# Performance work log

Measured on AMD Instinct MI355X. Metric: run time of the kernel, lower is better.

The kernel has to match this reference:

```python
import jax, jax.numpy as jnp
import numpy as np

N_NODES = 100000
N_EDGES = 1250000
D_FEAT = 64


def setup_inputs() -> dict:
    key = jax.random.key(0)
    k1, k2 = jax.random.split(key)
    x = jax.random.normal(k1, (N_NODES, D_FEAT), dtype=jnp.float32)
    edge_index = jax.random.randint(k2, (2, N_EDGES), 0, N_NODES, dtype=jnp.int64)
    return {"t": 0, "x": x, "edge_index": edge_index}


def reference(t, x, edge_index):
    # LGConv(normalize=False): out[i] = sum_{(j->i) in E} x[j]
    # adj_t SpMM expressed as gather + segment-sum scatter.
    src = edge_index[0]  # source/neighbor nodes
    dst = edge_index[1]  # destination nodes
    msgs = x[src]  # [E, D] gather
    out = jax.ops.segment_sum(msgs, dst, num_segments=N_NODES)  # [N, D]
    return out
```

## Files before the change

kernel.cpp:

```cpp
#include <hip/hip_runtime.h>

#define N_NODES 100000
#define N_EDGES 1250000
#define D_FEAT 64

#define NB_SHIFT 7
#define NODES_PER_B 128
#define N_BUCKETS ((N_NODES + NODES_PER_B - 1) / NODES_PER_B)
#define TROW (N_BUCKETS + 1)
#define NB_PAD 1024
#define MAX_BUCKET_EDGES 2048
#define SRC_BITS 17
#define SRC_MASK ((1u << SRC_BITS) - 1u)

#define CH 4992
#define NCH ((N_EDGES + CH - 1) / CH)
#define NCHP 256

__global__ __launch_bounds__(256) void lgconv_scatter(
    const float* __restrict__ x, const int* __restrict__ src,
    const int* __restrict__ dst, float* __restrict__ out) {
    int tid  = blockIdx.x * blockDim.x + threadIdx.x;
    int edge = tid >> 4;
    int f4   = (tid & 15) << 2;
    if (edge >= N_EDGES) return;
    int s = src[edge], d = dst[edge];
    const float4 v = *reinterpret_cast<const float4*>(x + (size_t)s * D_FEAT + f4);
    float* o = out + (size_t)d * D_FEAT + f4;
    unsafeAtomicAdd(o + 0, v.x); unsafeAtomicAdd(o + 1, v.y);
    unsafeAtomicAdd(o + 2, v.z); unsafeAtomicAdd(o + 3, v.w);
}

__device__ __forceinline__ unsigned short f2bf(float f) {
    unsigned int u = __float_as_uint(f);
    return (unsigned short)((u + 0x7FFFu + ((u >> 16) & 1u)) >> 16);
}
__device__ __forceinline__ float bflo(unsigned int p) {
    return __uint_as_float(p << 16);
}
__device__ __forceinline__ float bfhi(unsigned int p) {
    return __uint_as_float(p & 0xFFFF0000u);
}

__device__ __forceinline__ int wscan_incl(int v) {
    const int lane = threadIdx.x & 63;
#pragma unroll
    for (int off = 1; off < 64; off <<= 1) {
        int u = __shfl_up(v, off, 64);
        if (lane >= off) v += u;
    }
    return v;
}

template <bool CONV>
__global__ __launch_bounds__(1024) void k1_sort(
    const float* __restrict__ x, unsigned short* __restrict__ xb,
    const int* __restrict__ src, const int* __restrict__ dst,
    unsigned int* __restrict__ bins, unsigned short* __restrict__ tableT) {
    __shared__ int hist[NB_PAD];
    __shared__ int scanBase[NB_PAD];
    __shared__ int cur[NB_PAD];
    __shared__ int wsum[16];
    __shared__ unsigned int stage[CH];
    const int t    = threadIdx.x;
    const int c    = blockIdx.x;
    const int base = c * CH;
    const int cnt  = min(CH, N_EDGES - base);
    const int lane = t & 63;
    const int wid  = t >> 6;

    if (CONV) {
        const int F4 = N_NODES * D_FEAT / 4;
        for (int i = c * 1024 + t; i < F4; i += NCH * 1024) {
            float4 v = reinterpret_cast<const float4*>(x)[i];
            ushort4 o;
            o.x = f2bf(v.x); o.y = f2bf(v.y); o.z = f2bf(v.z); o.w = f2bf(v.w);
            reinterpret_cast<ushort4*>(xb)[i] = o;
        }
    }

    hist[t] = 0; cur[t] = 0;
    __syncthreads();
    for (int i = t; i < cnt; i += 1024)
        atomicAdd(&hist[dst[base + i] >> NB_SHIFT], 1);
    __syncthreads();

    int v = hist[t];
    int s = wscan_incl(v);
    if (lane == 63) wsum[wid] = s;
    __syncthreads();
    if (t < 16) {
        int w  = wsum[t];
        int ws = wscan_incl(w);
        wsum[t] = ws;
    }
    __syncthreads();
    int incl = s + (wid ? wsum[wid - 1] : 0);
    scanBase[t] = incl - v;
    __syncthreads();

    if (t < TROW) tableT[(size_t)t * NCHP + c] = (unsigned short)scanBase[t];

    for (int i = t; i < cnt; i += 1024) {
        int d = dst[base + i], sv = src[base + i];
        int b = d >> NB_SHIFT;
        unsigned int packed = ((unsigned int)(d & (NODES_PER_B - 1)) << SRC_BITS)
                            | (unsigned int)sv;
        int pos = scanBase[b] + atomicAdd(&cur[b], 1);
        stage[pos] = packed;
    }
    __syncthreads();
    for (int i = t; i < cnt; i += 1024) bins[base + i] = stage[i];
}

template <bool BF>
__global__ __launch_bounds__(512) void k2_accum(
    const float* __restrict__ x, const unsigned short* __restrict__ xb,
    const unsigned int* __restrict__ bins, const unsigned short* __restrict__ tableT,
    float* __restrict__ out) {
    __shared__ int            startA[512];
    __shared__ unsigned short lenA[512];
    __shared__ int            destB[512];
    __shared__ unsigned int   raw[MAX_BUCKET_EDGES];
    __shared__ unsigned int   srcs[MAX_BUCKET_EDGES];
    __shared__ int cntArr[NODES_PER_B];
    __shared__ int nodeOff[NODES_PER_B + 1];
    __shared__ int curN[NODES_PER_B];
    __shared__ int wsum[8];
    const int t    = threadIdx.x;
    const int b    = blockIdx.x;
    const int lane = t & 63;
    const int wid  = t >> 6;

    int st = 0, len = 0;
    if (t < NCH) {
        st  = tableT[(size_t)b * NCHP + t];
        len = (int)tableT[(size_t)(b + 1) * NCHP + t] - st;
    }
    startA[t] = st;
    lenA[t]   = (unsigned short)len;
    if (t < NODES_PER_B) cntArr[t] = 0;
    int s = wscan_incl(len);
    if (lane == 63) wsum[wid] = s;
    __syncthreads();
    if (t < 8) {
        int w  = wsum[t];
        int ws = wscan_incl(w);
        wsum[t] = ws;
    }
    __syncthreads();
    int incl = s + (wid ? wsum[wid - 1] : 0);
    destB[t] = incl - len;
    int cntTot = wsum[7];
    if (cntTot > MAX_BUCKET_EDGES) cntTot = MAX_BUCKET_EDGES;
    __syncthreads();

    {
        const int cj = t >> 3;
        const int jj = t & 7;
        for (int c0 = 0; c0 < NCH; c0 += 64) {
            int c = c0 + cj;
            if (c < NCH) {
                int l = lenA[c], s0 = startA[c], db = destB[c];
                const unsigned int* p = bins + (size_t)c * CH + s0;
                for (int q = jj; q < l; q += 8) raw[db + q] = p[q];
            }
        }
    }
    __syncthreads();

    for (int i = t; i < cntTot; i += 512)
        atomicAdd(&cntArr[raw[i] >> SRC_BITS], 1);
    __syncthreads();
    int v2 = (t < NODES_PER_B) ? cntArr[t] : 0;
    int s2 = wscan_incl(v2);
    if (t < NODES_PER_B && lane == 63) wsum[wid] = s2;
    __syncthreads();
    if (t < NODES_PER_B) {
        int excl = s2 + ((wid == 1) ? wsum[0] : 0) - v2;
        nodeOff[t] = excl;
        curN[t]    = excl;
    }
    if (t == 0) nodeOff[NODES_PER_B] = cntTot;
    __syncthreads();
    for (int i = t; i < cntTot; i += 512) {
        unsigned int p = raw[i];
        int pos = atomicAdd(&curN[p >> SRC_BITS], 1);
        srcs[pos] = p & SRC_MASK;
    }
    __syncthreads();

    if (BF) {
        int f0 = (t & 7) << 3;
        for (int g = 0; g < NODES_PER_B / 64; ++g) {
            int local = g * 64 + (t >> 3);
            int node  = b * NODES_PER_B + local;
            int beg = nodeOff[local], end = nodeOff[local + 1];
            float a0=0,a1=0,a2=0,a3=0,a4=0,a5=0,a6=0,a7=0;
            int k = beg;
            for (; k + 3 < end; k += 4) {
                const uint4 u0 = *reinterpret_cast<const uint4*>(
                    xb + (size_t)srcs[k] * D_FEAT + f0);
                const uint4 u1 = *reinterpret_cast<const uint4*>(
                    xb + (size_t)srcs[k + 1] * D_FEAT + f0);
                const uint4 u2 = *reinterpret_cast<const uint4*>(
                    xb + (size_t)srcs[k + 2] * D_FEAT + f0);
                const uint4 u3 = *reinterpret_cast<const uint4*>(
                    xb + (size_t)srcs[k + 3] * D_FEAT + f0);
                a0 += bflo(u0.x) + bflo(u1.x) + bflo(u2.x) + bflo(u3.x);
                a1 += bfhi(u0.x) + bfhi(u1.x) + bfhi(u2.x) + bfhi(u3.x);
                a2 += bflo(u0.y) + bflo(u1.y) + bflo(u2.y) + bflo(u3.y);
                a3 += bfhi(u0.y) + bfhi(u1.y) + bfhi(u2.y) + bfhi(u3.y);
                a4 += bflo(u0.z) + bflo(u1.z) + bflo(u2.z) + bflo(u3.z);
                a5 += bfhi(u0.z) + bfhi(u1.z) + bfhi(u2.z) + bfhi(u3.z);
                a6 += bflo(u0.w) + bflo(u1.w) + bflo(u2.w) + bflo(u3.w);
                a7 += bfhi(u0.w) + bfhi(u1.w) + bfhi(u2.w) + bfhi(u3.w);
            }
            for (; k < end; ++k) {
                const uint4 u = *reinterpret_cast<const uint4*>(
                    xb + (size_t)srcs[k] * D_FEAT + f0);
                a0 += bflo(u.x); a1 += bfhi(u.x);
                a2 += bflo(u.y); a3 += bfhi(u.y);
                a4 += bflo(u.z); a5 += bfhi(u.z);
                a6 += bflo(u.w); a7 += bfhi(u.w);
            }
            if (node < N_NODES) {
                float* op = out + (size_t)node * D_FEAT + f0;
                *reinterpret_cast<float4*>(op)     = make_float4(a0, a1, a2, a3);
                *reinterpret_cast<float4*>(op + 4) = make_float4(a4, a5, a6, a7);
            }
        }
    } else {
        int lane4 = (t & 15) << 2;
        for (int g = 0; g < NODES_PER_B / 32; ++g) {
            int local = g * 32 + (t >> 4);
            int node  = b * NODES_PER_B + local;
            int beg = nodeOff[local], end = nodeOff[local + 1];
            float4 acc = make_float4(0.f, 0.f, 0.f, 0.f);
            int k = beg;
            for (; k + 1 < end; k += 2) {
                unsigned int i0 = srcs[k], i1 = srcs[k + 1];
                const float4 a = *reinterpret_cast<const float4*>(x + (size_t)i0 * D_FEAT + lane4);
                const float4 c = *reinterpret_cast<const float4*>(x + (size_t)i1 * D_FEAT + lane4);
                acc.x += a.x + c.x; acc.y += a.y + c.y;
                acc.z += a.z + c.z; acc.w += a.w + c.w;
            }
            if (k < end) {
                unsigned int i0 = srcs[k];
                const float4 a = *reinterpret_cast<const float4*>(x + (size_t)i0 * D_FEAT + lane4);
                acc.x += a.x; acc.y += a.y; acc.z += a.z; acc.w += a.w;
            }
            if (node < N_NODES)
                *reinterpret_cast<float4*>(out + (size_t)node * D_FEAT + lane4) = acc;
        }
    }
}

extern "C" void kernel_launch(void* const* d_in, const int* in_sizes, int n_in,
                              void* d_out, int out_size, void* d_ws, size_t ws_size,
                              hipStream_t stream) {
    const float* x   = (const float*)d_in[1];
    const int*   ei  = (const int*)d_in[2];
    const int*   src = ei;
    const int*   dst = ei + N_EDGES;
    float*       out = (float*)d_out;

    const size_t tabBytes = (size_t)TROW * NCHP * sizeof(unsigned short);
    const size_t binBytes = (size_t)N_EDGES * sizeof(unsigned int);
    const size_t xbOff    = (binBytes + tabBytes + 15) & ~(size_t)15;
    const size_t needA    = xbOff + (size_t)N_NODES * D_FEAT * sizeof(unsigned short);
    const size_t needB    = binBytes + tabBytes;

    if (ws_size >= needA) {
        unsigned int*   bins   = (unsigned int*)d_ws;
        unsigned short* tableT = (unsigned short*)((char*)d_ws + binBytes);
        unsigned short* xb     = (unsigned short*)((char*)d_ws + xbOff);
        k1_sort<true><<<NCH, 1024, 0, stream>>>(x, xb, src, dst, bins, tableT);
        k2_accum<true><<<N_BUCKETS, 512, 0, stream>>>(x, xb, bins, tableT, out);
    } else if (ws_size >= needB) {
        unsigned int*   bins   = (unsigned int*)d_ws;
        unsigned short* tableT = (unsigned short*)((char*)d_ws + binBytes);
        k1_sort<false><<<NCH, 1024, 0, stream>>>(x, nullptr, src, dst, bins, tableT);
        k2_accum<false><<<N_BUCKETS, 512, 0, stream>>>(x, nullptr, bins, tableT, out);
    } else {
        hipMemsetAsync(out, 0, (size_t)out_size * sizeof(float), stream);
        const int total = N_EDGES * 16;
        lgconv_scatter<<<(total + 255) / 256, 256, 0, stream>>>(x, src, dst, out);
    }
}
```

Measured before the change: 134.5 us.

## Halve bucket size and split each node's neighbor list across two thread groups

```diff
diff --git a/kernel.cpp b/kernel.cpp
--- a/kernel.cpp
+++ b/kernel.cpp
@@ -4,12 +4,12 @@
 #define N_EDGES 1250000
 #define D_FEAT 64
 
-#define NB_SHIFT 7
-#define NODES_PER_B 128
+#define NB_SHIFT 6
+#define NODES_PER_B 64
 #define N_BUCKETS ((N_NODES + NODES_PER_B - 1) / NODES_PER_B)
 #define TROW (N_BUCKETS + 1)
-#define NB_PAD 1024
-#define MAX_BUCKET_EDGES 2048
+#define NB_PAD 2048
+#define MAX_BUCKET_EDGES 1280
 #define SRC_BITS 17
 #define SRC_MASK ((1u << SRC_BITS) - 1u)
 
@@ -79,14 +79,16 @@
         }
     }
 
-    hist[t] = 0; cur[t] = 0;
+    hist[t] = 0; hist[t + 1024] = 0;
+    cur[t]  = 0; cur[t + 1024]  = 0;
     __syncthreads();
     for (int i = t; i < cnt; i += 1024)
         atomicAdd(&hist[dst[base + i] >> NB_SHIFT], 1);
     __syncthreads();
 
-    int v = hist[t];
-    int s = wscan_incl(v);
+    int v0 = hist[2 * t], v1 = hist[2 * t + 1];
+    int pv = v0 + v1;
+    int s  = wscan_incl(pv);
     if (lane == 63) wsum[wid] = s;
     __syncthreads();
     if (t < 16) {
@@ -96,10 +98,13 @@
     }
     __syncthreads();
     int incl = s + (wid ? wsum[wid - 1] : 0);
-    scanBase[t] = incl - v;
-    __syncthreads();
-
-    if (t < TROW) tableT[(size_t)t * NCHP + c] = (unsigned short)scanBase[t];
+    int eb   = incl - pv;
+    scanBase[2 * t]     = eb;
+    scanBase[2 * t + 1] = eb + v0;
+    __syncthreads();
+
+    for (int i = t; i < TROW; i += 1024)
+        tableT[(size_t)i * NCHP + c] = (unsigned short)scanBase[i];
 
     for (int i = t; i < cnt; i += 1024) {
         int d = dst[base + i], sv = src[base + i];
@@ -156,14 +161,14 @@
     __syncthreads();
 
     {
-        const int cj = t >> 3;
-        const int jj = t & 7;
-        for (int c0 = 0; c0 < NCH; c0 += 64) {
+        const int cj = t >> 2;
+        const int jj = t & 3;
+        for (int c0 = 0; c0 < NCH; c0 += 128) {
             int c = c0 + cj;
             if (c < NCH) {
                 int l = lenA[c], s0 = startA[c], db = destB[c];
                 const unsigned int* p = bins + (size_t)c * CH + s0;
-                for (int q = jj; q < l; q += 8) raw[db + q] = p[q];
+                for (int q = jj; q < l; q += 4) raw[db + q] = p[q];
             }
         }
     }
@@ -172,16 +177,13 @@
     for (int i = t; i < cntTot; i += 512)
         atomicAdd(&cntArr[raw[i] >> SRC_BITS], 1);
     __syncthreads();
-    int v2 = (t < NODES_PER_B) ? cntArr[t] : 0;
-    int s2 = wscan_incl(v2);
-    if (t < NODES_PER_B && lane == 63) wsum[wid] = s2;
-    __syncthreads();
     if (t < NODES_PER_B) {
-        int excl = s2 + ((wid == 1) ? wsum[0] : 0) - v2;
-        nodeOff[t] = excl;
-        curN[t]    = excl;
-    }
-    if (t == 0) nodeOff[NODES_PER_B] = cntTot;
+        int v2 = cntArr[t];
+        int s2 = wscan_incl(v2);
+        nodeOff[t] = s2 - v2;
+        curN[t]    = s2 - v2;
+        if (t == 0) nodeOff[NODES_PER_B] = cntTot;
+    }
     __syncthreads();
     for (int i = t; i < cntTot; i += 512) {
         unsigned int p = raw[i];
@@ -191,14 +193,18 @@
     __syncthreads();
 
     if (BF) {
-        int f0 = (t & 7) << 3;
-        for (int g = 0; g < NODES_PER_B / 64; ++g) {
-            int local = g * 64 + (t >> 3);
+        const int f0  = (t & 7) << 3;
+        const int grp = (t >> 3) & 1;
+        for (int g = 0; g < NODES_PER_B / 32; ++g) {
+            int local = g * 32 + (t >> 4);
             int node  = b * NODES_PER_B + local;
             int beg = nodeOff[local], end = nodeOff[local + 1];
+            int half = (end - beg + 1) >> 1;
+            int b0 = grp ? (beg + half) : beg;
+            int e0 = grp ? end : (beg + half);
             float a0=0,a1=0,a2=0,a3=0,a4=0,a5=0,a6=0,a7=0;
-            int k = beg;
-            for (; k + 3 < end; k += 4) {
+            int k = b0;
+            for (; k + 3 < e0; k += 4) {
                 const uint4 u0 = *reinterpret_cast<const uint4*>(
                     xb + (size_t)srcs[k] * D_FEAT + f0);
                 const uint4 u1 = *reinterpret_cast<const uint4*>(
@@ -216,7 +222,7 @@
                 a6 += bflo(u0.w) + bflo(u1.w) + bflo(u2.w) + bflo(u3.w);
                 a7 += bfhi(u0.w) + bfhi(u1.w) + bfhi(u2.w) + bfhi(u3.w);
             }
-            for (; k < end; ++k) {
+            for (; k < e0; ++k) {
                 const uint4 u = *reinterpret_cast<const uint4*>(
                     xb + (size_t)srcs[k] * D_FEAT + f0);
                 a0 += bflo(u.x); a1 += bfhi(u.x);
@@ -224,7 +230,11 @@
                 a4 += bflo(u.z); a5 += bfhi(u.z);
                 a6 += bflo(u.w); a7 += bfhi(u.w);
             }
-            if (node < N_NODES) {
+            a0 += __shfl_xor(a0, 8, 64); a1 += __shfl_xor(a1, 8, 64);
+            a2 += __shfl_xor(a2, 8, 64); a3 += __shfl_xor(a3, 8, 64);
+            a4 += __shfl_xor(a4, 8, 64); a5 += __shfl_xor(a5, 8, 64);
+            a6 += __shfl_xor(a6, 8, 64); a7 += __shfl_xor(a7, 8, 64);
+            if (grp == 0 && node < N_NODES) {
                 float* op = out + (size_t)node * D_FEAT + f0;
                 *reinterpret_cast<float4*>(op)     = make_float4(a0, a1, a2, a3);
                 *reinterpret_cast<float4*>(op + 4) = make_float4(a4, a5, a6, a7);
```

New measurement: 136.2 us. Within noise of the previous version (+1.2%).

## Split bf16 feature table into quarter slabs and gather per quarter with lane reduction

Applied to the files above, without the earlier changes.

```diff
diff --git a/kernel.cpp b/kernel.cpp
--- a/kernel.cpp
+++ b/kernel.cpp
@@ -16,6 +16,12 @@
 #define CH 4992
 #define NCH ((N_EDGES + CH - 1) / CH)
 #define NCHP 256
+
+#define QFEAT 16
+#define QS_US4 (N_NODES * 4)
+#define QS_US  (N_NODES * QFEAT)
+
+typedef float f32x4 __attribute__((ext_vector_type(4)));
 
 __global__ __launch_bounds__(256) void lgconv_scatter(
     const float* __restrict__ x, const int* __restrict__ src,
@@ -75,7 +81,9 @@
             float4 v = reinterpret_cast<const float4*>(x)[i];
             ushort4 o;
             o.x = f2bf(v.x); o.y = f2bf(v.y); o.z = f2bf(v.z); o.w = f2bf(v.w);
-            reinterpret_cast<ushort4*>(xb)[i] = o;
+            int node = i >> 4, j = i & 15;
+            int q = j >> 2, w = j & 3;
+            reinterpret_cast<ushort4*>(xb)[(size_t)q * QS_US4 + node * 4 + w] = o;
         }
     }
 
@@ -91,8 +99,7 @@
     __syncthreads();
     if (t < 16) {
         int w  = wsum[t];
-        int ws = wscan_incl(w);
-        wsum[t] = ws;
+        wsum[t] = wscan_incl(w);
     }
     __syncthreads();
     int incl = s + (wid ? wsum[wid - 1] : 0);
@@ -134,8 +141,8 @@
 
     int st = 0, len = 0;
     if (t < NCH) {
-        st  = tableT[(size_t)b * NCHP + t];
-        len = (int)tableT[(size_t)(b + 1) * NCHP + t] - st;
+        st  = __builtin_nontemporal_load(tableT + (size_t)b * NCHP + t);
+        len = (int)__builtin_nontemporal_load(tableT + (size_t)(b + 1) * NCHP + t) - st;
     }
     startA[t] = st;
     lenA[t]   = (unsigned short)len;
@@ -145,8 +152,7 @@
     __syncthreads();
     if (t < 8) {
         int w  = wsum[t];
-        int ws = wscan_incl(w);
-        wsum[t] = ws;
+        wsum[t] = wscan_incl(w);
     }
     __syncthreads();
     int incl = s + (wid ? wsum[wid - 1] : 0);
@@ -163,7 +169,8 @@
             if (c < NCH) {
                 int l = lenA[c], s0 = startA[c], db = destB[c];
                 const unsigned int* p = bins + (size_t)c * CH + s0;
-                for (int q = jj; q < l; q += 8) raw[db + q] = p[q];
+                for (int q = jj; q < l; q += 8)
+                    raw[db + q] = __builtin_nontemporal_load(p + q);
             }
         }
     }
@@ -191,44 +198,56 @@
     __syncthreads();
 
     if (BF) {
-        int f0 = (t & 7) << 3;
-        for (int g = 0; g < NODES_PER_B / 64; ++g) {
-            int local = g * 64 + (t >> 3);
-            int node  = b * NODES_PER_B + local;
-            int beg = nodeOff[local], end = nodeOff[local + 1];
-            float a0=0,a1=0,a2=0,a3=0,a4=0,a5=0,a6=0,a7=0;
-            int k = beg;
-            for (; k + 3 < end; k += 4) {
-                const uint4 u0 = *reinterpret_cast<const uint4*>(
-                    xb + (size_t)srcs[k] * D_FEAT + f0);
-                const uint4 u1 = *reinterpret_cast<const uint4*>(
-                    xb + (size_t)srcs[k + 1] * D_FEAT + f0);
-                const uint4 u2 = *reinterpret_cast<const uint4*>(
-                    xb + (size_t)srcs[k + 2] * D_FEAT + f0);
-                const uint4 u3 = *reinterpret_cast<const uint4*>(
-                    xb + (size_t)srcs[k + 3] * D_FEAT + f0);
-                a0 += bflo(u0.x) + bflo(u1.x) + bflo(u2.x) + bflo(u3.x);
-                a1 += bfhi(u0.x) + bfhi(u1.x) + bfhi(u2.x) + bfhi(u3.x);
-                a2 += bflo(u0.y) + bflo(u1.y) + bflo(u2.y) + bflo(u3.y);
-                a3 += bfhi(u0.y) + bfhi(u1.y) + bfhi(u2.y) + bfhi(u3.y);
-                a4 += bflo(u0.z) + bflo(u1.z) + bflo(u2.z) + bflo(u3.z);
-                a5 += bfhi(u0.z) + bfhi(u1.z) + bfhi(u2.z) + bfhi(u3.z);
-                a6 += bflo(u0.w) + bflo(u1.w) + bflo(u2.w) + bflo(u3.w);
-                a7 += bfhi(u0.w) + bfhi(u1.w) + bfhi(u2.w) + bfhi(u3.w);
+        const int fl  = t & 1;
+        const int grp = (t >> 1) & 3;
+        const int sub = t >> 3;
+        for (int q = 0; q < 4; ++q) {
+            const unsigned short* xq = xb + (size_t)q * QS_US;
+            for (int g = 0; g < 2; ++g) {
+                int local = g * 64 + sub;
+                int node  = b * NODES_PER_B + local;
+                int beg = nodeOff[local], end = nodeOff[local + 1];
+                float a0=0,a1=0,a2=0,a3=0,a4=0,a5=0,a6=0,a7=0;
+                int k = beg + grp;
+                for (; k + 4 < end; k += 8) {
+                    const uint4 u0 = *reinterpret_cast<const uint4*>(
+                        xq + (size_t)srcs[k] * QFEAT + fl * 8);
+                    const uint4 u1 = *reinterpret_cast<const uint4*>(
+                        xq + (size_t)srcs[k + 4] * QFEAT + fl * 8);
+                    a0 += bflo(u0.x) + bflo(u1.x);
+                    a1 += bfhi(u0.x) + bfhi(u1.x);
+                    a2 += bflo(u0.y) + bflo(u1.y);
+                    a3 += bfhi(u0.y) + bfhi(u1.y);
+                    a4 += bflo(u0.z) + bflo(u1.z);
+                    a5 += bfhi(u0.z) + bfhi(u1.z);
+                    a6 += bflo(u0.w) + bflo(u1.w);
+                    a7 += bfhi(u0.w) + bfhi(u1.w);
+                }
+                for (; k < end; k += 4) {
+                    const uint4 u = *reinterpret_cast<const uint4*>(
+                        xq + (size_t)srcs[k] * QFEAT + fl * 8);
+                    a0 += bflo(u.x); a1 += bfhi(u.x);
+                    a2 += bflo(u.y); a3 += bfhi(u.y);
+                    a4 += bflo(u.z); a5 += bfhi(u.z);
+                    a6 += bflo(u.w); a7 += bfhi(u.w);
+                }
+                a0 += __shfl_xor(a0, 2, 64); a1 += __shfl_xor(a1, 2, 64);
+                a2 += __shfl_xor(a2, 2, 64); a3 += __shfl_xor(a3, 2, 64);
+                a4 += __shfl_xor(a4, 2, 64); a5 += __shfl_xor(a5, 2, 64);
+                a6 += __shfl_xor(a6, 2, 64); a7 += __shfl_xor(a7, 2, 64);
+                a0 += __shfl_xor(a0, 4, 64); a1 += __shfl_xor(a1, 4, 64);
+                a2 += __shfl_xor(a2, 4, 64); a3 += __shfl_xor(a3, 4, 64);
+                a4 += __shfl_xor(a4, 4, 64); a5 += __shfl_xor(a5, 4, 64);
+                a6 += __shfl_xor(a6, 4, 64); a7 += __shfl_xor(a7, 4, 64);
+                if (grp == 0 && node < N_NODES) {
+                    float* op = out + (size_t)node * D_FEAT + q * QFEAT + fl * 8;
+                    f32x4 w0 = {a0, a1, a2, a3};
+                    f32x4 w1 = {a4, a5, a6, a7};
+                    __builtin_nontemporal_store(w0, reinterpret_cast<f32x4*>(op));
+                    __builtin_nontemporal_store(w1, reinterpret_cast<f32x4*>(op + 4));
+                }
             }
-            for (; k < end; ++k) {
-                const uint4 u = *reinterpret_cast<const uint4*>(
-                    xb + (size_t)srcs[k] * D_FEAT + f0);
-                a0 += bflo(u.x); a1 += bfhi(u.x);
-                a2 += bflo(u.y); a3 += bfhi(u.y);
-                a4 += bflo(u.z); a5 += bfhi(u.z);
-                a6 += bflo(u.w); a7 += bfhi(u.w);
-            }
-            if (node < N_NODES) {
-                float* op = out + (size_t)node * D_FEAT + f0;
-                *reinterpret_cast<float4*>(op)     = make_float4(a0, a1, a2, a3);
-                *reinterpret_cast<float4*>(op + 4) = make_float4(a4, a5, a6, a7);
-            }
+            __syncthreads();
         }
     } else {
         int lane4 = (t & 15) << 2;
@@ -283,7 +302,7 @@
         k1_sort<false><<<NCH, 1024, 0, stream>>>(x, nullptr, src, dst, bins, tableT);
         k2_accum<false><<<N_BUCKETS, 512, 0, stream>>>(x, nullptr, bins, tableT, out);
     } else {
-        hipMemsetAsync(out, 0, (size_t)out_size * sizeof(float), stream);
+        (void)hipMemsetAsync(out, 0, (size_t)out_size * sizeof(float), stream);
         const int total = N_EDGES * 16;
         lgconv_scatter<<<(total + 255) / 256, 256, 0, stream>>>(x, src, dst, out);
     }
```

New measurement: 140.8 us. 4.7% more time.
